# Optimization experiments

Measured on AMD Instinct MI355X. Metric: run time of the kernel, lower is better.

Reference implementation:

```python
import jax, jax.numpy as jnp
import numpy as np

B, T, C, H = 4, 2048, 1024, 16
HD = C // H  # head dim = 64


def setup_inputs() -> dict:
    key = jax.random.key(0)
    k1, k2, k3 = jax.random.split(key, 3)
    scale_in = 1.0 / np.sqrt(C)
    return {
        "x": jax.random.normal(k1, (B, T, C), dtype=jnp.float32),
        "W_attn": jax.random.normal(k2, (C, 3 * C), dtype=jnp.float32) * scale_in,
        "b_attn": jnp.zeros((3 * C,), dtype=jnp.float32),
        "W_proj": jax.random.normal(k3, (C, C), dtype=jnp.float32) * scale_in,
        "b_proj": jnp.zeros((C,), dtype=jnp.float32),
    }


def reference(x, W_attn, b_attn, W_proj, b_proj):
    b, t, c = x.shape
    qkv = x @ W_attn + b_attn                      # [B,T,3C]
    q, k, v = jnp.split(qkv, 3, axis=-1)
    # [B,T,C] -> [B,H,T,HD]
    def heads(z):
        return z.reshape(b, t, H, HD).transpose(0, 2, 1, 3)
    q, k, v = heads(q), heads(k), heads(v)
    att = jnp.einsum("bhqd,bhkd->bhqk", q, k) / jnp.sqrt(jnp.float32(HD))
    causal = jnp.tril(jnp.ones((t, t), dtype=bool))
    att = jnp.where(causal, att, -jnp.inf)
    att = jax.nn.softmax(att, axis=-1)             # dropout p=0 -> identity
    y = jnp.einsum("bhqk,bhkd->bhqd", att, v)      # [B,H,T,HD]
    y = y.transpose(0, 2, 1, 3).reshape(b, t, c)   # [B,T,C]
    return y @ W_proj + b_proj
```

## Files before the change

kernel.cpp:

```cpp
#include <hip/hip_runtime.h>
#include <hip/hip_bf16.h>

typedef unsigned int u32;
typedef unsigned short u16;
typedef __bf16 bf16x8 __attribute__((ext_vector_type(8)));
typedef float f32x4 __attribute__((ext_vector_type(4)));
typedef _Float16 f16;
typedef _Float16 f16x2 __attribute__((ext_vector_type(2)));
typedef _Float16 f16x4 __attribute__((ext_vector_type(4)));

#define B_ 4
#define T_ 2048
#define C_ 1024
#define H_ 16
#define HD_ 64
#define M_ (B_*T_)
#define N3C (3*C_)
#define N2C (2*C_)

__device__ __forceinline__ u16 f2bf(float f) {
  u32 u = __builtin_bit_cast(u32, f);
  u = (u + 0x7fffu + ((u >> 16) & 1u)) >> 16;
  return (u16)u;
}

#define GLD16(gp, lp) __builtin_amdgcn_global_load_lds( \
    (const __attribute__((address_space(1))) u32*)(gp), \
    (__attribute__((address_space(3))) u32*)(lp), 16, 0, 0)

#if __has_builtin(__builtin_amdgcn_exp2f)
#define EXP2F(x) __builtin_amdgcn_exp2f(x)
#else
#define EXP2F(x) exp2f(x)
#endif

__global__ __launch_bounds__(256) void prep(
    const float* __restrict__ x, const float* __restrict__ Wa,
    const float* __restrict__ Wp,
    u16* __restrict__ xb, u16* __restrict__ W1t, u16* __restrict__ W2t) {
  __shared__ float t[32][33];
  const int blk = blockIdx.x, tid = threadIdx.x;
  if (blk < 8192) {
    int i = blk * 256 + tid;
    float4 v = ((const float4*)x)[i];
    ushort4 o;
    o.x = f2bf(v.x); o.y = f2bf(v.y); o.z = f2bf(v.z); o.w = f2bf(v.w);
    ((ushort4*)xb)[i] = o;
    return;
  }
  const float* W; u16* Wt; int Ndim, id;
  if (blk < 8192 + 3072) { W = Wa; Wt = W1t; Ndim = N3C; id = blk - 8192; }
  else                   { W = Wp; Wt = W2t; Ndim = C_;  id = blk - 11264; }
  const int nt = Ndim / 32;
  const int n0 = (id % nt) * 32, k0 = (id / nt) * 32;
  const int tx = tid & 31, ty = tid >> 5;
  #pragma unroll
  for (int i = ty; i < 32; i += 8)
    t[i][tx] = W[(long)(k0 + i) * Ndim + n0 + tx];
  __syncthreads();
  #pragma unroll
  for (int i = ty; i < 32; i += 8)
    Wt[(long)(n0 + i) * C_ + k0 + tx] = f2bf(t[tx][i]);
}

__global__ __launch_bounds__(256) void gemm_qkv(
    const u16* __restrict__ A, const u16* __restrict__ Bt,
    const float* __restrict__ bias, u16* __restrict__ qkout,
    f16* __restrict__ vt) {
  __shared__ u16 As[128 * 64];
  __shared__ u16 Bs[128 * 64];
  const int tid = threadIdx.x;
  const int wave = tid >> 6, lane = tid & 63;
  const int wm = wave >> 1, wn = wave & 1;
  const int l15 = lane & 15, quad = lane >> 4;
  const int rA = lane >> 3, cxor = (lane & 7) ^ rA;
  const long rowA0 = (long)blockIdx.x * 128;
  const long colB0 = (long)blockIdx.y * 128;
  const int K = C_;

  f32x4 acc[4][4] = {};

  const u16* Ag = A + (rowA0 + wave * 32 + rA) * K + cxor * 8;
  const u16* Bg = Bt + (colB0 + wave * 32 + rA) * K + cxor * 8;
  u16* Asw = &As[(wave * 32) * 64];
  u16* Bsw = &Bs[(wave * 32) * 64];

  const int fbase = l15 * 64 + ((quad ^ (l15 & 3)) << 3) + (((l15 >> 2) & 1) << 5);
  const int aA0 = wm * 4096 + fbase, aA1 = aA0 ^ 32;
  const int bA0 = wn * 4096 + fbase, bA1 = bA0 ^ 32;

  for (int k0 = 0; k0 < K; k0 += 64) {
    #pragma unroll
    for (int j = 0; j < 4; ++j) {
      GLD16(Ag + (long)j * 8 * K + k0, Asw + j * 8 * 64);
      GLD16(Bg + (long)j * 8 * K + k0, Bsw + j * 8 * 64);
    }
    __syncthreads();
    #pragma unroll
    for (int kk = 0; kk < 2; ++kk) {
      const int ai = kk ? aA1 : aA0;
      const int bi = kk ? bA1 : bA0;
      bf16x8 af[4], bfr[4];
      #pragma unroll
      for (int mt = 0; mt < 4; ++mt)
        af[mt] = *(const bf16x8*)&As[ai + mt * 1024];
      #pragma unroll
      for (int nt = 0; nt < 4; ++nt)
        bfr[nt] = *(const bf16x8*)&Bs[bi + nt * 1024];
      #pragma unroll
      for (int mt = 0; mt < 4; ++mt)
        #pragma unroll
        for (int nt = 0; nt < 4; ++nt)
          acc[mt][nt] = __builtin_amdgcn_mfma_f32_16x16x32_bf16(
              af[mt], bfr[nt], acc[mt][nt], 0, 0, 0);
    }
    __syncthreads();
  }

  float bl[4];
  #pragma unroll
  for (int nt = 0; nt < 4; ++nt)
    bl[nt] = bias[colB0 + wn * 64 + nt * 16 + l15];

  const bool vmode = (colB0 >= N2C);
  #pragma unroll
  for (int mt = 0; mt < 4; ++mt) {
    long row = rowA0 + wm * 64 + mt * 16 + quad * 4;
    #pragma unroll
    for (int nt = 0; nt < 4; ++nt) {
      long col = colB0 + wn * 64 + nt * 16 + l15;
      float v0 = acc[mt][nt][0] + bl[nt];
      float v1 = acc[mt][nt][1] + bl[nt];
      float v2 = acc[mt][nt][2] + bl[nt];
      float v3 = acc[mt][nt][3] + bl[nt];
      if (!vmode) {
        qkout[(row + 0) * N2C + col] = f2bf(v0);
        qkout[(row + 1) * N2C + col] = f2bf(v1);
        qkout[(row + 2) * N2C + col] = f2bf(v2);
        qkout[(row + 3) * N2C + col] = f2bf(v3);
      } else {
        int cv = (int)(col - N2C);
        int hh = cv >> 6, dd = cv & 63;
        int bb = (int)(row >> 11);
        long t = row & 2047;
        f16x2 lo = __builtin_bit_cast(f16x2, __builtin_amdgcn_cvt_pkrtz(v0, v1));
        f16x2 hi = __builtin_bit_cast(f16x2, __builtin_amdgcn_cvt_pkrtz(v2, v3));
        f16x4 w; w[0] = lo[0]; w[1] = lo[1]; w[2] = hi[0]; w[3] = hi[1];
        *(f16x4*)&vt[(((long)bb * H_ + hh) * HD_ + dd) * T_ + t] = w;
      }
    }
  }
}

__global__ __launch_bounds__(256) void gemm_proj(
    const u16* __restrict__ A, const u16* __restrict__ Bt,
    const float* __restrict__ bias, float* __restrict__ Cout) {
  __shared__ u16 As[128 * 64];
  __shared__ u16 Bs[64 * 64];
  const int tid = threadIdx.x;
  const int wave = tid >> 6, lane = tid & 63;
  const int l15 = lane & 15, quad = lane >> 4;
  const int rA = lane >> 3, cxor = (lane & 7) ^ rA;
  const long rowA0 = (long)blockIdx.x * 128;
  const long colB0 = (long)blockIdx.y * 64;
  const int K = C_;

  f32x4 acc[2][4] = {};

  const u16* Ag = A + (rowA0 + wave * 32 + rA) * K + cxor * 8;
  const u16* Bg = Bt + (colB0 + wave * 16 + rA) * K + cxor * 8;
  u16* Asw = &As[(wave * 32) * 64];
  u16* Bsw = &Bs[(wave * 16) * 64];

  const int fbase = l15 * 64 + ((quad ^ (l15 & 3)) << 3) + (((l15 >> 2) & 1) << 5);
  const int aA0 = wave * 2048 + fbase, aA1 = aA0 ^ 32;
  const int bA0 = fbase, bA1 = bA0 ^ 32;

  for (int k0 = 0; k0 < K; k0 += 64) {
    #pragma unroll
    for (int j = 0; j < 4; ++j)
      GLD16(Ag + (long)j * 8 * K + k0, Asw + j * 8 * 64);
    #pragma unroll
    for (int j = 0; j < 2; ++j)
      GLD16(Bg + (long)j * 8 * K + k0, Bsw + j * 8 * 64);
    __syncthreads();
    #pragma unroll
    for (int kk = 0; kk < 2; ++kk) {
      const int ai = kk ? aA1 : aA0;
      const int bi = kk ? bA1 : bA0;
      bf16x8 af[2], bfr[4];
      #pragma unroll
      for (int mt = 0; mt < 2; ++mt)
        af[mt] = *(const bf16x8*)&As[ai + mt * 1024];
      #pragma unroll
      for (int nt = 0; nt < 4; ++nt)
        bfr[nt] = *(const bf16x8*)&Bs[bi + nt * 1024];
      #pragma unroll
      for (int mt = 0; mt < 2; ++mt)
        #pragma unroll
        for (int nt = 0; nt < 4; ++nt)
          acc[mt][nt] = __builtin_amdgcn_mfma_f32_16x16x32_bf16(
              af[mt], bfr[nt], acc[mt][nt], 0, 0, 0);
    }
    __syncthreads();
  }

  float bl[4];
  #pragma unroll
  for (int nt = 0; nt < 4; ++nt)
    bl[nt] = bias[colB0 + nt * 16 + l15];
  #pragma unroll
  for (int mt = 0; mt < 2; ++mt) {
    long row = rowA0 + wave * 32 + mt * 16 + quad * 4;
    #pragma unroll
    for (int nt = 0; nt < 4; ++nt) {
      long col = colB0 + nt * 16 + l15;
      #pragma unroll
      for (int r = 0; r < 4; ++r)
        Cout[(row + r) * C_ + col] = acc[mt][nt][r] + bl[nt];
    }
  }
}

__global__ __launch_bounds__(256, 5) void flash_attn(
    const u16* __restrict__ qk, const f16* __restrict__ vt,
    u16* __restrict__ yb) {
  __shared__ u16 KsF[2 * 64 * 64];
  __shared__ f16 VsF[2 * 64 * 64];
  const int l = blockIdx.x;
  const int bh = l & 63;
  const int qt = 31 - (l >> 6);
  const int b = bh >> 4, h = bh & 15;
  const int tid = threadIdx.x, wave = tid >> 6, lane = tid & 63;
  const int l15 = lane & 15, quad = lane >> 4;
  const int rA = lane >> 3, cxor = (lane & 7) ^ rA;

  const u16* Qb = qk + (long)b * T_ * N2C + h * HD_;
  const f16* Vbase = vt + (long)bh * HD_ * T_;
  const u16* Kb0 = Qb + C_ + (long)(wave * 16 + rA) * N2C + cxor * 8;
  const f16* Vb0 = Vbase + (long)(wave * 16 + rA) * T_ + cxor * 8;

  u16* ksw0 = &KsF[(wave * 16) * 64];
  u16* ksw1 = &KsF[4096 + (wave * 16) * 64];
  f16* vsw0 = &VsF[(wave * 16) * 64];
  f16* vsw1 = &VsF[4096 + (wave * 16) * 64];

  const int kA0 = l15 * 64 + ((quad ^ (l15 & 3)) << 3) + (((l15 >> 2) & 1) << 5);
  const int kA1 = kA0 ^ 32;
  const int vA0 = l15 * 64 + (((quad >> 1) ^ (l15 & 7)) << 3) + ((quad & 1) << 2);

  const float cs = 0.125f * 1.44269504088896340736f;

#define FA_TILE(KT, BUF) do {                                                  \
    __syncthreads();                         \
    if ((KT) + 1 < nKT) {                                                      \
      u16* kd = (BUF) ? ksw0 : ksw1;                                           \
      f16* vd = (BUF) ? vsw0 : vsw1;                                           \
      GLD16(kp, kd);                                                           \
      GLD16(kp + 8 * N2C, kd + 8 * 64);                                        \
      GLD16(vp, vd);                                                           \
      GLD16(vp + 8 * T_, vd + 8 * 64);                                         \
      kp += 64 * N2C;                                                          \
      vp += 64;                                                                \
    }                                                                          \
    f32x4 St[4] = {};                                                          \
    _Pragma("unroll")                                                          \
    for (int kk = 0; kk < 2; ++kk) {                                           \
      bf16x8 qf = kk ? bq1 : bq0;                                              \
      const int ki = ((kk ? kA1 : kA0)) + (BUF) * 4096;                        \
      _Pragma("unroll")                                                        \
      for (int mt = 0; mt < 4; ++mt) {                                         \
        bf16x8 kf = *(const bf16x8*)&KsF[ki + mt * 1024];                      \
        St[mt] = __builtin_amdgcn_mfma_f32_16x16x32_bf16(kf, qf, St[mt],       \
                                                         0, 0, 0);             \
      }                                                                        \
    }                                                                          \
    if ((KT) == qt) {                                                          \
      _Pragma("unroll")                                                        \
      for (int mt = 0; mt < 4; ++mt)                                           \
        _Pragma("unroll")                                                      \
        for (int r = 0; r < 4; ++r)                                            \
          if (mt * 16 + quad * 4 + r > wave * 16 + l15)                        \
            St[mt][r] = -__builtin_inff();                                     \
    }                                                                          \
    float ps = 0.f;                                                            \
    f16x4 pf[4];                                                               \
    _Pragma("unroll")                                                          \
    for (int mt = 0; mt < 4; ++mt) {                                           \
      float p0 = EXP2F(__builtin_fmaf(St[mt][0], cs, nref));                   \
      float p1 = EXP2F(__builtin_fmaf(St[mt][1], cs, nref));                   \
      float p2 = EXP2F(__builtin_fmaf(St[mt][2], cs, nref));                   \
      float p3 = EXP2F(__builtin_fmaf(St[mt][3], cs, nref));                   \
      ps += (p0 + p1) + (p2 + p3);                                             \
      f16x2 lo = __builtin_bit_cast(f16x2, __builtin_amdgcn_cvt_pkrtz(p0, p1));\
      f16x2 hi = __builtin_bit_cast(f16x2, __builtin_amdgcn_cvt_pkrtz(p2, p3));\
      pf[mt][0] = lo[0]; pf[mt][1] = lo[1];                                    \
      pf[mt][2] = hi[0]; pf[mt][3] = hi[1];                                    \
    }                                                                          \
    li += ps;                                                                  \
    _Pragma("unroll")                                                          \
    for (int kc = 0; kc < 4; ++kc) {                                           \
      const int vi = (vA0 ^ (kc << 4)) + (BUF) * 4096;                         \
      _Pragma("unroll")                                                        \
      for (int dt = 0; dt < 4; ++dt) {                                         \
        f16x4 vf = *(const f16x4*)&VsF[vi + dt * 1024];                        \
        o[dt] = __builtin_amdgcn_mfma_f32_16x16x16f16(vf, pf[kc], o[dt],       \
                                                      0, 0, 0);               \
      }                                                                        \
    }                                                                          \
  } while (0)

  const int nKT = qt + 1;
  const int qrow = qt * 64 + wave * 16 + l15;
  const bf16x8 bq0 = *(const bf16x8*)&Qb[(long)qrow * N2C + quad * 8];
  const bf16x8 bq1 = *(const bf16x8*)&Qb[(long)qrow * N2C + 32 + quad * 8];

  float qq = 0.f;
  #pragma unroll
  for (int j = 0; j < 8; ++j) {
    float a = (float)bq0[j], bv = (float)bq1[j];
    qq = __builtin_fmaf(a, a, qq);
    qq = __builtin_fmaf(bv, bv, qq);
  }
  qq += __shfl_xor(qq, 16);
  qq += __shfl_xor(qq, 32);
  const float nref = -qq * cs;

  const u16* kp = Kb0;
  const f16* vp = Vb0;

  GLD16(kp, ksw0);
  GLD16(kp + 8 * N2C, ksw0 + 8 * 64);
  GLD16(vp, vsw0);
  GLD16(vp + 8 * T_, vsw0 + 8 * 64);
  kp += 64 * N2C;
  vp += 64;

  float li = 0.f;
  f32x4 o[4] = {};

  int kt = 0;
  #pragma unroll 1
  for (; kt + 1 < nKT; kt += 2) {
    FA_TILE(kt, 0);
    FA_TILE(kt + 1, 1);
  }
  if (nKT & 1) FA_TILE(nKT - 1, 0);

  li += __shfl_xor(li, 16);
  li += __shfl_xor(li, 32);
  float inv = 1.f / li;
  #pragma unroll
  for (int dt = 0; dt < 4; ++dt) {
    ushort4 w;
    w.x = f2bf(o[dt][0] * inv);
    w.y = f2bf(o[dt][1] * inv);
    w.z = f2bf(o[dt][2] * inv);
    w.w = f2bf(o[dt][3] * inv);
    *(ushort4*)&yb[((long)b * T_ + qrow) * C_ + h * HD_ + dt * 16 + quad * 4] = w;
  }
#undef FA_TILE
}

extern "C" void kernel_launch(void* const* d_in, const int* in_sizes, int n_in,
                              void* d_out, int out_size, void* d_ws, size_t ws_size,
                              hipStream_t stream) {
  const float* x      = (const float*)d_in[0];
  const float* W_attn = (const float*)d_in[1];
  const float* b_attn = (const float*)d_in[2];
  const float* W_proj = (const float*)d_in[3];
  const float* b_proj = (const float*)d_in[4];
  float* out = (float*)d_out;

  char* ws = (char*)d_ws;
  u16* xb   = (u16*)(ws);
  u16* W1t  = (u16*)(ws + 16777216);
  u16* W2t  = (u16*)(ws + 23068672);
  u16* qkb  = (u16*)(ws + 25165824);
  f16* vtb  = (f16*)(ws + 58720256);
  u16* yb   = (u16*)(ws + 75497472);

  prep<<<dim3(12288), dim3(256), 0, stream>>>(x, W_attn, W_proj, xb, W1t, W2t);
  gemm_qkv<<<dim3(M_ / 128, N3C / 128), dim3(256), 0, stream>>>(
      xb, W1t, b_attn, qkb, vtb);
  flash_attn<<<dim3(2048), dim3(256), 0, stream>>>(qkb, vtb, yb);
  gemm_proj<<<dim3(M_ / 128, C_ / 64), dim3(256), 0, stream>>>(
      yb, W2t, b_proj, out);
}
```

Measured before the change: 238.4 us.

## Use two waves per attention block with each wave owning 32 query rows

The flash-attention block shrinks from four waves to two. Each wave now processes two 16-row query groups, so every K and V fragment read from LDS feeds twice as many MFMAs. The aim is to cut LDS read traffic and the number of waves per block that contend at barriers. In exchange each wave holds twice the registers (two sets of accumulators and scores). Each thread also issues twice the global-to-LDS loads, and the launch-bounds occupancy hint is dropped.

```diff
diff --git a/kernel.cpp b/kernel.cpp
--- a/kernel.cpp
+++ b/kernel.cpp
@@ -222,7 +222,7 @@
   }
 }
 
-__global__ __launch_bounds__(256, 5) void flash_attn(
+__global__ __launch_bounds__(128) void flash_attn(
     const u16* __restrict__ qk, const f16* __restrict__ vt,
     u16* __restrict__ yb) {
   __shared__ u16 KsF[2 * 64 * 64];
@@ -237,13 +237,13 @@
 
   const u16* Qb = qk + (long)b * T_ * N2C + h * HD_;
   const f16* Vbase = vt + (long)bh * HD_ * T_;
-  const u16* Kb0 = Qb + C_ + (long)(wave * 16 + rA) * N2C + cxor * 8;
-  const f16* Vb0 = Vbase + (long)(wave * 16 + rA) * T_ + cxor * 8;
-
-  u16* ksw0 = &KsF[(wave * 16) * 64];
-  u16* ksw1 = &KsF[4096 + (wave * 16) * 64];
-  f16* vsw0 = &VsF[(wave * 16) * 64];
-  f16* vsw1 = &VsF[4096 + (wave * 16) * 64];
+  const u16* Kb0 = Qb + C_ + (long)(wave * 32 + rA) * N2C + cxor * 8;
+  const f16* Vb0 = Vbase + (long)(wave * 32 + rA) * T_ + cxor * 8;
+
+  u16* ksw0 = &KsF[(wave * 32) * 64];
+  u16* ksw1 = &KsF[4096 + (wave * 32) * 64];
+  f16* vsw0 = &VsF[(wave * 32) * 64];
+  f16* vsw1 = &VsF[4096 + (wave * 32) * 64];
 
   const int kA0 = l15 * 64 + ((quad ^ (l15 & 3)) << 3) + (((l15 >> 2) & 1) << 5);
   const int kA1 = kA0 ^ 32;
@@ -258,86 +258,107 @@
       f16* vd = (BUF) ? vsw0 : vsw1;                                           \
       GLD16(kp, kd);                                                           \
       GLD16(kp + 8 * N2C, kd + 8 * 64);                                        \
+      GLD16(kp + 16 * N2C, kd + 16 * 64);                                      \
+      GLD16(kp + 24 * N2C, kd + 24 * 64);                                      \
       GLD16(vp, vd);                                                           \
       GLD16(vp + 8 * T_, vd + 8 * 64);                                         \
+      GLD16(vp + 16 * T_, vd + 16 * 64);                                       \
+      GLD16(vp + 24 * T_, vd + 24 * 64);                                       \
       kp += 64 * N2C;                                                          \
       vp += 64;                                                                \
     }                                                                          \
-    f32x4 St[4] = {};                                                          \
+    f32x4 St[2][4] = {};                                                       \
     _Pragma("unroll")                                                          \
     for (int kk = 0; kk < 2; ++kk) {                                           \
-      bf16x8 qf = kk ? bq1 : bq0;                                              \
       const int ki = ((kk ? kA1 : kA0)) + (BUF) * 4096;                        \
       _Pragma("unroll")                                                        \
       for (int mt = 0; mt < 4; ++mt) {                                         \
         bf16x8 kf = *(const bf16x8*)&KsF[ki + mt * 1024];                      \
-        St[mt] = __builtin_amdgcn_mfma_f32_16x16x32_bf16(kf, qf, St[mt],       \
-                                                         0, 0, 0);             \
+        St[0][mt] = __builtin_amdgcn_mfma_f32_16x16x32_bf16(                   \
+            kf, bq[0][kk], St[0][mt], 0, 0, 0);                                \
+        St[1][mt] = __builtin_amdgcn_mfma_f32_16x16x32_bf16(                   \
+            kf, bq[1][kk], St[1][mt], 0, 0, 0);                                \
       }                                                                        \
     }                                                                          \
     if ((KT) == qt) {                                                          \
       _Pragma("unroll")                                                        \
-      for (int mt = 0; mt < 4; ++mt)                                           \
+      for (int g = 0; g < 2; ++g)                                              \
         _Pragma("unroll")                                                      \
-        for (int r = 0; r < 4; ++r)                                            \
-          if (mt * 16 + quad * 4 + r > wave * 16 + l15)                        \
-            St[mt][r] = -__builtin_inff();                                     \
+        for (int mt = 0; mt < 4; ++mt)                                         \
+          _Pragma("unroll")                                                    \
+          for (int r = 0; r < 4; ++r)                                          \
+            if (mt * 16 + quad * 4 + r > wave * 32 + g * 16 + l15)             \
+              St[g][mt][r] = -__builtin_inff();                                \
     }                                                                          \
-    float ps = 0.f;                                                            \
-    f16x4 pf[4];                                                               \
+    f16x4 pf[2][4];                                                            \
     _Pragma("unroll")                                                          \
-    for (int mt = 0; mt < 4; ++mt) {                                           \
-      float p0 = EXP2F(__builtin_fmaf(St[mt][0], cs, nref));                   \
-      float p1 = EXP2F(__builtin_fmaf(St[mt][1], cs, nref));                   \
-      float p2 = EXP2F(__builtin_fmaf(St[mt][2], cs, nref));                   \
-      float p3 = EXP2F(__builtin_fmaf(St[mt][3], cs, nref));                   \
-      ps += (p0 + p1) + (p2 + p3);                                             \
-      f16x2 lo = __builtin_bit_cast(f16x2, __builtin_amdgcn_cvt_pkrtz(p0, p1));\
-      f16x2 hi = __builtin_bit_cast(f16x2, __builtin_amdgcn_cvt_pkrtz(p2, p3));\
-      pf[mt][0] = lo[0]; pf[mt][1] = lo[1];                                    \
-      pf[mt][2] = hi[0]; pf[mt][3] = hi[1];                                    \
+    for (int g = 0; g < 2; ++g) {                                              \
+      float ps = 0.f;                                                          \
+      _Pragma("unroll")                                                        \
+      for (int mt = 0; mt < 4; ++mt) {                                         \
+        float p0 = EXP2F(__builtin_fmaf(St[g][mt][0], cs, nref[g]));           \
+        float p1 = EXP2F(__builtin_fmaf(St[g][mt][1], cs, nref[g]));           \
+        float p2 = EXP2F(__builtin_fmaf(St[g][mt][2], cs, nref[g]));           \
+        float p3 = EXP2F(__builtin_fmaf(St[g][mt][3], cs, nref[g]));           \
+        ps += (p0 + p1) + (p2 + p3);                                           \
+        f16x2 lo = __builtin_bit_cast(f16x2,                                   \
+                                      __builtin_amdgcn_cvt_pkrtz(p0, p1));     \
+        f16x2 hi = __builtin_bit_cast(f16x2,                                   \
+                                      __builtin_amdgcn_cvt_pkrtz(p2, p3));     \
+        pf[g][mt][0] = lo[0]; pf[g][mt][1] = lo[1];                            \
+        pf[g][mt][2] = hi[0]; pf[g][mt][3] = hi[1];                            \
+      }                                                                        \
+      li[g] += ps;                                                             \
     }                                                                          \
-    li += ps;                                                                  \
     _Pragma("unroll")                                                          \
     for (int kc = 0; kc < 4; ++kc) {                                           \
       const int vi = (vA0 ^ (kc << 4)) + (BUF) * 4096;                         \
       _Pragma("unroll")                                                        \
       for (int dt = 0; dt < 4; ++dt) {                                         \
         f16x4 vf = *(const f16x4*)&VsF[vi + dt * 1024];                        \
-        o[dt] = __builtin_amdgcn_mfma_f32_16x16x16f16(vf, pf[kc], o[dt],       \
-                                                      0, 0, 0);               \
+        o[0][dt] = __builtin_amdgcn_mfma_f32_16x16x16f16(                      \
+            vf, pf[0][kc], o[0][dt], 0, 0, 0);                                 \
+        o[1][dt] = __builtin_amdgcn_mfma_f32_16x16x16f16(                      \
+            vf, pf[1][kc], o[1][dt], 0, 0, 0);                                 \
       }                                                                        \
     }                                                                          \
   } while (0)
 
   const int nKT = qt + 1;
-  const int qrow = qt * 64 + wave * 16 + l15;
-  const bf16x8 bq0 = *(const bf16x8*)&Qb[(long)qrow * N2C + quad * 8];
-  const bf16x8 bq1 = *(const bf16x8*)&Qb[(long)qrow * N2C + 32 + quad * 8];
-
-  float qq = 0.f;
-  #pragma unroll
-  for (int j = 0; j < 8; ++j) {
-    float a = (float)bq0[j], bv = (float)bq1[j];
-    qq = __builtin_fmaf(a, a, qq);
-    qq = __builtin_fmaf(bv, bv, qq);
-  }
-  qq += __shfl_xor(qq, 16);
-  qq += __shfl_xor(qq, 32);
-  const float nref = -qq * cs;
+  bf16x8 bq[2][2];
+  float nref[2], li[2] = {0.f, 0.f};
+  #pragma unroll
+  for (int g = 0; g < 2; ++g) {
+    const int qrow = qt * 64 + wave * 32 + g * 16 + l15;
+    bq[g][0] = *(const bf16x8*)&Qb[(long)qrow * N2C + quad * 8];
+    bq[g][1] = *(const bf16x8*)&Qb[(long)qrow * N2C + 32 + quad * 8];
+    float qq = 0.f;
+    #pragma unroll
+    for (int j = 0; j < 8; ++j) {
+      float a = (float)bq[g][0][j], bv = (float)bq[g][1][j];
+      qq = __builtin_fmaf(a, a, qq);
+      qq = __builtin_fmaf(bv, bv, qq);
+    }
+    qq += __shfl_xor(qq, 16);
+    qq += __shfl_xor(qq, 32);
+    nref[g] = -qq * cs;
+  }
 
   const u16* kp = Kb0;
   const f16* vp = Vb0;
 
   GLD16(kp, ksw0);
   GLD16(kp + 8 * N2C, ksw0 + 8 * 64);
+  GLD16(kp + 16 * N2C, ksw0 + 16 * 64);
+  GLD16(kp + 24 * N2C, ksw0 + 24 * 64);
   GLD16(vp, vsw0);
   GLD16(vp + 8 * T_, vsw0 + 8 * 64);
+  GLD16(vp + 16 * T_, vsw0 + 16 * 64);
+  GLD16(vp + 24 * T_, vsw0 + 24 * 64);
   kp += 64 * N2C;
   vp += 64;
 
-  float li = 0.f;
-  f32x4 o[4] = {};
+  f32x4 o[2][4] = {};
 
   int kt = 0;
   #pragma unroll 1
@@ -347,17 +368,21 @@
   }
   if (nKT & 1) FA_TILE(nKT - 1, 0);
 
-  li += __shfl_xor(li, 16);
-  li += __shfl_xor(li, 32);
-  float inv = 1.f / li;
-  #pragma unroll
-  for (int dt = 0; dt < 4; ++dt) {
-    ushort4 w;
-    w.x = f2bf(o[dt][0] * inv);
-    w.y = f2bf(o[dt][1] * inv);
-    w.z = f2bf(o[dt][2] * inv);
-    w.w = f2bf(o[dt][3] * inv);
-    *(ushort4*)&yb[((long)b * T_ + qrow) * C_ + h * HD_ + dt * 16 + quad * 4] = w;
+  #pragma unroll
+  for (int g = 0; g < 2; ++g) {
+    li[g] += __shfl_xor(li[g], 16);
+    li[g] += __shfl_xor(li[g], 32);
+    float inv = 1.f / li[g];
+    const long qrow = qt * 64 + wave * 32 + g * 16 + l15;
+    #pragma unroll
+    for (int dt = 0; dt < 4; ++dt) {
+      ushort4 w;
+      w.x = f2bf(o[g][dt][0] * inv);
+      w.y = f2bf(o[g][dt][1] * inv);
+      w.z = f2bf(o[g][dt][2] * inv);
+      w.w = f2bf(o[g][dt][3] * inv);
+      *(ushort4*)&yb[((long)b * T_ + qrow) * C_ + h * HD_ + dt * 16 + quad * 4] = w;
+    }
   }
 #undef FA_TILE
 }
@@ -383,7 +408,7 @@
   prep<<<dim3(12288), dim3(256), 0, stream>>>(x, W_attn, W_proj, xb, W1t, W2t);
   gemm_qkv<<<dim3(M_ / 128, N3C / 128), dim3(256), 0, stream>>>(
       xb, W1t, b_attn, qkb, vtb);
-  flash_attn<<<dim3(2048), dim3(256), 0, stream>>>(qkb, vtb, yb);
+  flash_attn<<<dim3(2048), dim3(128), 0, stream>>>(qkb, vtb, yb);
   gemm_proj<<<dim3(M_ / 128, C_ / 64), dim3(256), 0, stream>>>(
       yb, W2t, b_proj, out);
 }
```

New measurement: 240.3 us. About the same (+0.8%).
